# Performance work log

Measured on AMD Instinct MI355X. Metric: run time of the kernel, lower is better.

The kernel has to match this reference:

```python
import jax, jax.numpy as jnp
import numpy as np

DELAY = 4
SKIP = 2
NF = 8
HS = 256
EPS = 1e-5


def setup_inputs() -> dict:
    key = jax.random.key(0)
    ks = jax.random.split(key, 11)
    B, NP, NO, T = 16, 512, 512, 2048
    predictor = jax.random.normal(ks[0], (B, NP, T), dtype=jnp.float32)
    to_order = jax.random.normal(ks[1], (B, NO, T), dtype=jnp.float32)
    trilinear = jax.random.normal(ks[2], (NF, NO, NP), dtype=jnp.float32) / np.float32(np.sqrt(NP * NO))
    w_o = jax.random.normal(ks[3], (HS, NO), dtype=jnp.float32) / np.float32(np.sqrt(NO))
    b_o = jax.random.normal(ks[4], (HS,), dtype=jnp.float32) * 0.01
    w_p = jax.random.normal(ks[5], (HS, NP), dtype=jnp.float32) / np.float32(np.sqrt(NP))
    b_p = jax.random.normal(ks[6], (HS,), dtype=jnp.float32) * 0.01
    bn_gamma = jnp.ones((HS,), dtype=jnp.float32)
    bn_beta = jnp.zeros((HS,), dtype=jnp.float32)
    w_out = jax.random.normal(ks[7], (NF, HS), dtype=jnp.float32) / np.float32(np.sqrt(HS))
    b_out = jax.random.normal(ks[8], (NF,), dtype=jnp.float32) * 0.01
    return {"predictor": predictor, "to_order": to_order, "trilinear": trilinear,
            "w_o": w_o, "b_o": b_o, "w_p": w_p, "b_p": b_p,
            "bn_gamma": bn_gamma, "bn_beta": bn_beta, "w_out": w_out, "b_out": b_out}


def reference(predictor, to_order, trilinear, w_o, b_o, w_p, b_p, bn_gamma, bn_beta, w_out, b_out):
    B, NP, T = predictor.shape
    NO = to_order.shape[1]
    tot_latency = DELAY + SKIP * (NF - 1)
    T_r = T - tot_latency
    pred = predictor[:, :, :T_r]          # (B, np, Tr)
    too = to_order[:, :, DELAY:]          # (B, no, T - delay)
    # predictor_product[b,k,t,m] = sum_p pred[b,p,t] * trilinear[k,m,p]
    pp = jnp.einsum('bpt,kmp->bktm', pred, trilinear)           # (B, nf, Tr, no)
    win = jnp.stack([too[:, :, j * SKIP: j * SKIP + T_r] for j in range(NF)], axis=1)  # (B, nf, no, Tr)
    inner = jnp.einsum('bjmt,bktm->bjkt', win, pp)              # (B, nf, nf, Tr)
    # conv1d (kernel 1) heads
    o_proj = jnp.einsum('hm,bmt->bht', w_o, too) + b_o[None, :, None]    # (B, hs, T - delay)
    p_proj = jnp.einsum('hp,bpt->bht', w_p, pred) + b_p[None, :, None]   # (B, hs, Tr)
    o_win = jnp.stack([o_proj[:, :, j * SKIP: j * SKIP + T_r] for j in range(NF)], axis=1)  # (B, nf, hs, Tr)
    h = jax.nn.relu(o_win + p_proj[:, None])                    # (B, nf, hs, Tr)
    # BatchNorm1d (training-mode batch stats) over (B*nf, hs, Tr): stats over axes (0,1,3)
    mean = h.mean(axis=(0, 1, 3), keepdims=True)
    var = h.var(axis=(0, 1, 3), keepdims=True)
    h = (h - mean) * jax.lax.rsqrt(var + EPS) * bn_gamma[None, None, :, None] + bn_beta[None, None, :, None]
    head = jnp.einsum('kh,bjht->bjkt', w_out, h) + b_out[None, None, :, None]
    inner = inner + head
    log_probs = jax.nn.log_softmax(inner, axis=2)               # (B, nf, nf, Tr)
    correct = jnp.einsum('bjjt->bjt', log_probs)                # diagonal j == k
    return correct.mean(axis=2).mean(axis=0)                    # (nf,)
```

## Files before the change

### kernel.cpp

```cpp
#include <hip/hip_runtime.h>
#include <math.h>

constexpr int B_  = 16;
constexpr int NP_ = 512;
constexpr int NO_ = 512;
constexpr int T_  = 2048;
constexpr int NF_ = 8;
constexpr int HS_ = 256;
constexpr int TR_ = 2030;
constexpr int TO_ = 2044;
constexpr int OPLD_ = 2048;
constexpr float EPS_ = 1e-5f;

typedef short bf16x8 __attribute__((ext_vector_type(8)));
typedef float f32x16 __attribute__((ext_vector_type(16)));

__device__ __forceinline__ unsigned short f2bf(float f) {
  union { float f; unsigned int u; } v; v.f = f;
  unsigned int r = v.u + 0x7fffu + ((v.u >> 16) & 1u);
  return (unsigned short)(r >> 16);
}
__device__ __forceinline__ float bf2f(unsigned short u) {
  union { unsigned int u; float f; } v; v.u = ((unsigned int)u) << 16;
  return v.f;
}

typedef const __attribute__((address_space(1))) unsigned int* gas_u32;
typedef __attribute__((address_space(3))) unsigned int* las_u32;
__device__ __forceinline__ void gl16(const void* g, void* l) {
  __builtin_amdgcn_global_load_lds((gas_u32)g, (las_u32)l, 16, 0, 0);
}


__global__ __launch_bounds__(256) void transpose_cvt(
    const float* __restrict__ in, unsigned short* __restrict__ outb) {
  __shared__ float tile[64][65];
  const int c0 = blockIdx.x * 64;
  const int r0 = blockIdx.y * 64;
  const int b  = blockIdx.z;
  const float* ib = in + (size_t)b * 512 * 2048;
  unsigned short* ob = outb + (size_t)b * 2048 * 512;
  for (int i = threadIdx.x; i < 64 * 16; i += 256) {
    const int r = i >> 4, c4 = (i & 15) * 4;
    float4 v = *(const float4*)(ib + (size_t)(r0 + r) * 2048 + c0 + c4);
    tile[r][c4 + 0] = v.x; tile[r][c4 + 1] = v.y;
    tile[r][c4 + 2] = v.z; tile[r][c4 + 3] = v.w;
  }
  __syncthreads();
  for (int i = threadIdx.x; i < 64 * 8; i += 256) {
    const int c = i >> 3, r8 = (i & 7) * 8;
    unsigned int pk[4];
    #pragma unroll
    for (int e = 0; e < 4; ++e)
      pk[e] = (unsigned int)f2bf(tile[r8 + 2 * e][c]) |
              ((unsigned int)f2bf(tile[r8 + 2 * e + 1][c]) << 16);
    *(uint4*)(ob + (size_t)(c0 + c) * 512 + r0 + r8) = *(uint4*)pk;
  }
}

__global__ __launch_bounds__(256) void cvt_bf16(
    const float* __restrict__ in, unsigned short* __restrict__ out, int n) {
  const int i = (blockIdx.x * 256 + threadIdx.x) * 4;
  if (i < n) {
    float4 v = *(const float4*)(in + i);
    ushort4 o; o.x = f2bf(v.x); o.y = f2bf(v.y); o.z = f2bf(v.z); o.w = f2bf(v.w);
    *(ushort4*)(out + i) = o;
  }
}

__global__ __launch_bounds__(256, 2) void proj_mfma(
    const unsigned short* __restrict__ Wbf,
    const unsigned short* __restrict__ Xt,
    const float* __restrict__ bias,
    unsigned short* __restrict__ out,
    int Tlen, int toff) {
  __shared__ char smem[65536];
  char* const Ab[2] = { smem, smem + 16384 };
  char* const Bb[2] = { smem + 32768, smem + 49152 };
  const int tid = threadIdx.x;
  const int l = tid & 63, wv = tid >> 6;
  const int h = l >> 5, tl = l & 31;
  const int mq = wv >> 1, tq = wv & 1;
  const int t0 = blockIdx.x * 128;
  const int m0 = blockIdx.y * 128;
  const int b  = blockIdx.z;
  const unsigned short* Xb = Xt + (size_t)b * T_ * 512;

  int aSrc[4], bSrc[4], ldsO[4];
  #pragma unroll
  for (int i = 0; i < 4; ++i) {
    const int q = (wv << 8) + (i << 6) + l;
    const int r = q >> 3, c8s = (q & 7) ^ (r & 7);
    aSrc[i] = (m0 + r) * 512 + (c8s << 3);
    const int row = min(t0 + toff + r, T_ - 1);
    bSrc[i] = row * 512 + (c8s << 3);
    ldsO[i] = ((wv << 8) + (i << 6)) << 4;
  }

  f32x16 acc[2][2];
  #pragma unroll
  for (int i = 0; i < 2; ++i)
    #pragma unroll
    for (int jj = 0; jj < 2; ++jj)
      #pragma unroll
      for (int e = 0; e < 16; ++e) acc[i][jj][e] = 0.f;

  #pragma unroll
  for (int i = 0; i < 4; ++i) gl16(Wbf + aSrc[i], Ab[0] + ldsO[i]);
  #pragma unroll
  for (int i = 0; i < 4; ++i) gl16(Xb + bSrc[i], Bb[0] + ldsO[i]);
  asm volatile("s_waitcnt vmcnt(0)" ::: "memory");
  __builtin_amdgcn_s_barrier();

  #pragma unroll
  for (int ps = 0; ps < 8; ++ps) {
    const int cb = ps & 1;
    if (ps < 7) {
      const int p0 = (ps + 1) << 6;
      #pragma unroll
      for (int i = 0; i < 4; ++i) gl16(Wbf + p0 + aSrc[i], Ab[cb ^ 1] + ldsO[i]);
      #pragma unroll
      for (int i = 0; i < 4; ++i) gl16(Xb + p0 + bSrc[i], Bb[cb ^ 1] + ldsO[i]);
    }
    const unsigned short* As = (const unsigned short*)Ab[cb];
    const unsigned short* Bs = (const unsigned short*)Bb[cb];
    #pragma unroll
    for (int s = 0; s < 4; ++s) {
      const int k8 = 2 * s + h;
      bf16x8 af[2], bfr[2];
      #pragma unroll
      for (int mt = 0; mt < 2; ++mt) {
        const int rm = 64 * mq + 32 * mt + tl;
        af[mt] = *(const bf16x8*)(As + rm * 64 + ((k8 ^ (rm & 7)) << 3));
      }
      #pragma unroll
      for (int nt = 0; nt < 2; ++nt) {
        const int rt = 64 * tq + 32 * nt + tl;
        bfr[nt] = *(const bf16x8*)(Bs + rt * 64 + ((k8 ^ (rt & 7)) << 3));
      }
      #pragma unroll
      for (int mt = 0; mt < 2; ++mt)
        #pragma unroll
        for (int nt = 0; nt < 2; ++nt)
          acc[mt][nt] = __builtin_amdgcn_mfma_f32_32x32x16_bf16(
              af[mt], bfr[nt], acc[mt][nt], 0, 0, 0);
    }
    asm volatile("s_waitcnt vmcnt(0)" ::: "memory");
    __builtin_amdgcn_s_barrier();
  }
  #pragma unroll
  for (int mt = 0; mt < 2; ++mt)
    #pragma unroll
    for (int nt = 0; nt < 2; ++nt)
      #pragma unroll
      for (int r = 0; r < 16; ++r) {
        const int hs = m0 + 64 * mq + 32 * mt + (r & 3) + 8 * (r >> 2) + 4 * h;
        const int t  = t0 + 64 * tq + 32 * nt + tl;
        if (t < Tlen)
          out[((size_t)b * HS_ + hs) * OPLD_ + t] = f2bf(acc[mt][nt][r] + bias[hs]);
      }
}

__global__ __launch_bounds__(256, 2) void inner_mfma(
    const unsigned short* __restrict__ pred_t,
    const unsigned short* __restrict__ too_t,
    const unsigned short* __restrict__ tri_bf,
    float* __restrict__ inner) {
  __shared__ char smem[77824];
  char* const Pb[2] = { smem, smem + 16384 };
  char* const Tb[2] = { smem + 32768, smem + 49152 };
  char* const TOOM  = smem + 65536;
  char* const TAIL  = smem + 32768;
  const int tid = threadIdx.x;
  const int l = tid & 63, wv = tid >> 6;
  const int h = l >> 5, tl = l & 31;
  const int mh = wv & 1, th = wv >> 1;
  const int t0 = blockIdx.x * 128;
  const int kf0 = blockIdx.y * 2;
  const int b  = blockIdx.z;
  const unsigned short* predB = pred_t + (size_t)b * T_ * NP_;
  const unsigned short* tooB  = too_t  + (size_t)b * T_ * NO_;
  const unsigned short* triK  = tri_bf + (size_t)kf0 * NO_ * NP_;

  int pSrc[4], pLds[4];
  #pragma unroll
  for (int i = 0; i < 4; ++i) {
    const int q = (wv << 8) + (i << 6) + l;
    const int r = q >> 3, c8s = (q & 7) ^ (r & 7);
    pSrc[i] = (t0 + r) * NP_ + (c8s << 3);
    pLds[i] = ((wv << 8) + (i << 6)) << 4;
  }
  int tSrc[4], tLds[4];
  #pragma unroll
  for (int i = 0; i < 4; ++i) {
    const int q = (wv << 8) + (i << 6) + l;
    const int f = q >> 9, qq = q & 511;
    const int r = qq >> 3, c8s = (qq & 7) ^ (r & 7);
    tSrc[i] = f * (NO_ * NP_) + r * NP_ + (c8s << 3);
    tLds[i] = ((wv << 8) + (i << 6)) << 4;
  }
  int oSrc[3], oLds[3];
  #pragma unroll
  for (int i = 0; i < 3; ++i) {
    const int q = wv * 192 + (i << 6) + l;
    const int r = q >> 3, c8s = (q & 7) ^ (r & 7);
    oSrc[i] = (t0 + r) * NO_ + (c8s << 3);
    oLds[i] = (wv * 192 + (i << 6)) << 4;
  }
  int aSrcT[4], aLdsT[4];
  {
    const int ws = (wv >= 2) ? (wv - 2) : 0;
    #pragma unroll
    for (int i = 0; i < 4; ++i) {
      const int q = (ws << 8) + (i << 6) + l;
      const int r = 96 + (q >> 3), c8s = (q & 7) ^ (r & 7);
      aSrcT[i] = min(t0 + r, T_ - 1) * NO_ + (c8s << 3);
      aLdsT[i] = ((ws << 8) + (i << 6)) << 4;
    }
  }

  f32x16 Sacc[2][2];
  #pragma unroll
  for (int f = 0; f < 2; ++f)
    #pragma unroll
    for (int ct = 0; ct < 2; ++ct)
      #pragma unroll
      for (int e = 0; e < 16; ++e) Sacc[f][ct][e] = 0.f;

  for (int mc = 0; mc < 8; ++mc) {
    const int m0 = mc << 6;
    const int mOff = m0 * NP_;
    __builtin_amdgcn_s_barrier();
    #pragma unroll
    for (int i = 0; i < 3; ++i) gl16(tooB + m0 + oSrc[i], TOOM + oLds[i]);
    #pragma unroll
    for (int i = 0; i < 4; ++i) gl16(triK + mOff + tSrc[i], Tb[0] + tLds[i]);
    #pragma unroll
    for (int i = 0; i < 4; ++i) gl16(predB + pSrc[i], Pb[0] + pLds[i]);
    asm volatile("s_waitcnt vmcnt(0)" ::: "memory");
    __builtin_amdgcn_s_barrier();

    f32x16 Qacc[2][2];
    #pragma unroll
    for (int f = 0; f < 2; ++f)
      #pragma unroll
      for (int nt = 0; nt < 2; ++nt)
        #pragma unroll
        for (int e = 0; e < 16; ++e) Qacc[f][nt][e] = 0.f;

    #pragma unroll
    for (int ps = 0; ps < 8; ++ps) {
      const int cb = ps & 1;
      if (ps < 7) {
        const int p1 = (ps + 1) << 6;
        #pragma unroll
        for (int i = 0; i < 4; ++i)
          gl16(triK + mOff + p1 + tSrc[i], Tb[cb ^ 1] + tLds[i]);
        #pragma unroll
        for (int i = 0; i < 4; ++i)
          gl16(predB + p1 + pSrc[i], Pb[cb ^ 1] + pLds[i]);
      }
      const unsigned short* predS = (const unsigned short*)Pb[cb];
      const unsigned short* triS  = (const unsigned short*)Tb[cb];
      __builtin_amdgcn_s_setprio(1);
      #pragma unroll
      for (int s = 0; s < 4; ++s) {
        const int k8 = 2 * s + h;
        const int swz = (k8 ^ (tl & 7)) << 3;
        bf16x8 a[2], bp[2];
        #pragma unroll
        for (int f = 0; f < 2; ++f)
          a[f] = *(const bf16x8*)(triS + f * 4096 + ((mh << 5) + tl) * 64 + swz);
        #pragma unroll
        for (int nt = 0; nt < 2; ++nt)
          bp[nt] = *(const bf16x8*)(predS + ((th << 6) + (nt << 5) + tl) * 64 + swz);
        #pragma unroll
        for (int f = 0; f < 2; ++f)
          #pragma unroll
          for (int nt = 0; nt < 2; ++nt)
            Qacc[f][nt] = __builtin_amdgcn_mfma_f32_32x32x16_bf16(
                a[f], bp[nt], Qacc[f][nt], 0, 0, 0);
      }
      __builtin_amdgcn_s_setprio(0);
      if (ps == 7 && wv >= 2) {
        #pragma unroll
        for (int i = 0; i < 4; ++i)
          gl16(tooB + m0 + aSrcT[i], TAIL + aLdsT[i]);
      }
      asm volatile("s_waitcnt vmcnt(0)" ::: "memory");
      __builtin_amdgcn_s_barrier();
    }
    #pragma unroll
    for (int f = 0; f < 2; ++f)
      #pragma unroll
      for (int nt = 0; nt < 2; ++nt) {
        unsigned short* QSw = (unsigned short*)(Pb[f] + (((th << 1) + nt) << 12));
        #pragma unroll
        for (int rp = 0; rp < 8; ++rp) {
          const int r = rp << 1;
          const int m = (mh << 5) + (r & 3) + ((r >> 2) << 3) + (h << 2);
          const int c8 = m >> 3, ml = m & 7;
          const int rX = (tl & 24) | ((tl ^ c8) & 7);
          const unsigned int pk = (unsigned int)f2bf(Qacc[f][nt][r]) |
                                  ((unsigned int)f2bf(Qacc[f][nt][r + 1]) << 16);
          *(unsigned int*)(QSw + (((c8 << 5) + rX) << 3) + ml) = pk;
        }
      }
    asm volatile("s_waitcnt lgkmcnt(0)" ::: "memory");
    __builtin_amdgcn_s_barrier();
    #pragma unroll
    for (int s = 0; s < 4; ++s) {
      const int k8 = 2 * s + h;
      bf16x8 atoo[2];
      #pragma unroll
      for (int ct = 0; ct < 2; ++ct) {
        const int rbase = (wv + ct) << 5;
        const int rr = rbase + tl;
        const unsigned short* tb = (rbase < 96)
            ? (const unsigned short*)TOOM + (size_t)rr * 64
            : (const unsigned short*)TAIL + (size_t)(rr - 96) * 64;
        atoo[ct] = *(const bf16x8*)(tb + ((k8 ^ (rr & 7)) << 3));
      }
      const int rqX = (tl & 24) | ((tl ^ k8) & 7);
      #pragma unroll
      for (int f = 0; f < 2; ++f) {
        const bf16x8 bq = *(const bf16x8*)((const unsigned short*)(Pb[f] + (wv << 12)) +
                                           (((k8 << 5) + rqX) << 3));
        #pragma unroll
        for (int ct = 0; ct < 2; ++ct)
          Sacc[f][ct] = __builtin_amdgcn_mfma_f32_32x32x16_bf16(atoo[ct], bq, Sacc[f][ct], 0, 0, 0);
      }
    }
  }
  __syncthreads();
  const int tglob = t0 + (wv << 5) + tl;
  float* SW = (float*)smem + (wv << 11);
  #pragma unroll
  for (int f = 0; f < 2; ++f) {
    #pragma unroll
    for (int ct = 0; ct < 2; ++ct)
      #pragma unroll
      for (int r = 0; r < 16; ++r) {
        const int cc = (ct << 5) + (r & 3) + ((r >> 2) << 3) + (h << 2);
        SW[(cc << 5) + tl] = Sacc[f][ct][r];
      }
    if (tglob < TR_) {
      #pragma unroll
      for (int jj = 0; jj < 4; ++jj) {
        const int j = (jj << 1) + h;
        const float v = SW[((tl + 4 + 2 * j) << 5) + tl];
        inner[(((size_t)b * NF_ + j) * NF_ + (kf0 + f)) * TR_ + tglob] = v;
      }
    }
  }
}

__global__ __launch_bounds__(256) void bn_stats(
    const unsigned short* __restrict__ op, const unsigned short* __restrict__ pp,
    float* __restrict__ partials) {
  const int hh = blockIdx.x, b = blockIdx.y;
  const unsigned short* oprow = op + ((size_t)b * HS_ + hh) * OPLD_;
  const unsigned short* pprow = pp + ((size_t)b * HS_ + hh) * OPLD_;
  float s = 0.f, s2 = 0.f;
  const int t8 = threadIdx.x * 8;
  if (t8 < TR_) {
    uint4 pv4 = *(const uint4*)(pprow + t8);
    uint4 ov[3];
    ov[0] = *(const uint4*)(oprow + t8);
    ov[1] = *(const uint4*)(oprow + t8 + 8);
    ov[2] = *(const uint4*)(oprow + t8 + 16);
    float ppf[8], opf[24];
    #pragma unroll
    for (int i = 0; i < 4; ++i) {
      const unsigned int u = (&pv4.x)[i];
      ppf[2 * i]     = bf2f((unsigned short)(u & 0xffffu));
      ppf[2 * i + 1] = bf2f((unsigned short)(u >> 16));
    }
    #pragma unroll
    for (int g = 0; g < 3; ++g)
      #pragma unroll
      for (int i = 0; i < 4; ++i) {
        const unsigned int u = (&ov[g].x)[i];
        opf[8 * g + 2 * i]     = bf2f((unsigned short)(u & 0xffffu));
        opf[8 * g + 2 * i + 1] = bf2f((unsigned short)(u >> 16));
      }
    #pragma unroll
    for (int e = 0; e < 8; ++e) {
      if (t8 + e < TR_) {
        #pragma unroll
        for (int j = 0; j < NF_; ++j) {
          float r = fmaxf(opf[e + 2 * j] + ppf[e], 0.f);
          s += r; s2 += r * r;
        }
      }
    }
  }
  __shared__ float red[256], red2[256];
  red[threadIdx.x] = s; red2[threadIdx.x] = s2;
  __syncthreads();
  for (int st = 128; st > 0; st >>= 1) {
    if (threadIdx.x < st) {
      red[threadIdx.x]  += red[threadIdx.x + st];
      red2[threadIdx.x] += red2[threadIdx.x + st];
    }
    __syncthreads();
  }
  if (threadIdx.x == 0) {
    partials[b * HS_ + hh]            = red[0];
    partials[B_ * HS_ + b * HS_ + hh] = red2[0];
  }
}

__global__ __launch_bounds__(256) void bn_finalize(
    const float* __restrict__ partials, const float* __restrict__ gamma,
    const float* __restrict__ beta, const float* __restrict__ w_out,
    const float* __restrict__ b_out, float* __restrict__ w_eff,
    float* __restrict__ cvec) {
  const int hh = threadIdx.x;
  float s = 0.f, s2 = 0.f;
  for (int b = 0; b < B_; ++b) {
    s  += partials[b * HS_ + hh];
    s2 += partials[B_ * HS_ + b * HS_ + hh];
  }
  const float cnt  = (float)B_ * NF_ * TR_;
  const float mean = s / cnt;
  const float var  = s2 / cnt - mean * mean;
  const float scale = gamma[hh] * rsqrtf(var + EPS_);
  const float shift = beta[hh] - mean * scale;
  #pragma unroll
  for (int k = 0; k < NF_; ++k) w_eff[k * HS_ + hh] = w_out[k * HS_ + hh] * scale;
  __shared__ float red[256];
  for (int k = 0; k < NF_; ++k) {
    red[hh] = w_out[k * HS_ + hh] * shift;
    __syncthreads();
    for (int st = 128; st > 0; st >>= 1) {
      if (hh < st) red[hh] += red[hh + st];
      __syncthreads();
    }
    if (hh == 0) cvec[k] = b_out[k] + red[0];
    __syncthreads();
  }
}

__global__ __launch_bounds__(256) void head_final(
    const unsigned short* __restrict__ op, const unsigned short* __restrict__ pp,
    const float* __restrict__ w_eff, const float* __restrict__ cvec,
    const float* __restrict__ inner, float* __restrict__ part3) {
  __shared__ float opS[144 * 20];
  __shared__ float ppS[128 * 20];
  __shared__ float weS[8][256];
  __shared__ float red[4][2];
  const int tid = threadIdx.x;
  const int tl = tid & 127, jp = tid >> 7;
  const int t0 = blockIdx.x * 128;
  const int b  = blockIdx.y;
  const int jh = blockIdx.z;
  for (int i = tid; i < 8 * 256; i += 256) weS[i >> 8][i & 255] = w_eff[i];
  float acc[2][8] = {};
  const unsigned short* opb = op + (size_t)b * HS_ * OPLD_;
  const unsigned short* ppb = pp + (size_t)b * HS_ * OPLD_;
  for (int hc = 0; hc < 16; ++hc) {
    const int h0 = hc << 4;
    __syncthreads();
    for (int idx = tid; idx < 288; idx += 256) {
      const int r = idx / 18, cc = (idx - r * 18) << 3;
      const int g = min(t0 + cc, OPLD_ - 8);
      uint4 v = *(const uint4*)(opb + (size_t)(h0 + r) * OPLD_ + g);
      #pragma unroll
      for (int e = 0; e < 4; ++e) {
        const unsigned int u = (&v.x)[e];
        opS[(cc + 2 * e) * 20 + r]     = bf2f((unsigned short)(u & 0xffffu));
        opS[(cc + 2 * e + 1) * 20 + r] = bf2f((unsigned short)(u >> 16));
      }
    }
    {
      const int r = tid >> 4, cc = (tid & 15) << 3;
      uint4 v = *(const uint4*)(ppb + (size_t)(h0 + r) * OPLD_ + t0 + cc);
      #pragma unroll
      for (int e = 0; e < 4; ++e) {
        const unsigned int u = (&v.x)[e];
        ppS[(cc + 2 * e) * 20 + r]     = bf2f((unsigned short)(u & 0xffffu));
        ppS[(cc + 2 * e + 1) * 20 + r] = bf2f((unsigned short)(u >> 16));
      }
    }
    __syncthreads();
    float pv[16];
    #pragma unroll
    for (int i = 0; i < 4; ++i) {
      float4 q = *(const float4*)(ppS + tl * 20 + 4 * i);
      pv[4 * i + 0] = q.x; pv[4 * i + 1] = q.y;
      pv[4 * i + 2] = q.z; pv[4 * i + 3] = q.w;
    }
    #pragma unroll
    for (int jj = 0; jj < 2; ++jj) {
      const int col = tl + 2 * ((jh << 2) + (jp << 1) + jj);
      #pragma unroll
      for (int i = 0; i < 4; ++i) {
        float4 ov = *(const float4*)(opS + col * 20 + 4 * i);
        #pragma unroll
        for (int e = 0; e < 4; ++e) {
          const float r = fmaxf((&ov.x)[e] + pv[4 * i + e], 0.f);
          #pragma unroll
          for (int k = 0; k < 8; ++k) acc[jj][k] += weS[k][h0 + 4 * i + e] * r;
        }
      }
    }
  }
  const int t = t0 + tl;
  float sj[2];
  #pragma unroll
  for (int jj = 0; jj < 2; ++jj) {
    if (t < TR_) {
      const int j = (jh << 2) + (jp << 1) + jj;
      float v[8]; float mx = -1e30f;
      #pragma unroll
      for (int k = 0; k < 8; ++k) {
        v[k] = acc[jj][k] + cvec[k] +
               inner[(((size_t)b * NF_ + j) * NF_ + k) * TR_ + t];
        mx = fmaxf(mx, v[k]);
      }
      float se = 0.f;
      #pragma unroll
      for (int k = 0; k < 8; ++k) se += expf(v[k] - mx);
      sj[jj] = v[j] - mx - logf(se);
    } else sj[jj] = 0.f;
  }
  #pragma unroll
  for (int jj = 0; jj < 2; ++jj)
    #pragma unroll
    for (int off = 32; off > 0; off >>= 1) sj[jj] += __shfl_down(sj[jj], off);
  if ((tid & 63) == 0) {
    const int wv = tid >> 6;
    #pragma unroll
    for (int jj = 0; jj < 2; ++jj) red[wv][jj] = sj[jj];
  }
  __syncthreads();
  if (tid < 4) {
    const int qp = tid >> 1, qj = tid & 1;
    const float s = red[2 * qp][qj] + red[2 * qp + 1][qj];
    const int j = (jh << 2) + (qp << 1) + qj;
    part3[(j * B_ + b) * 16 + blockIdx.x] = s;
  }
}

__global__ void final_out(const float* __restrict__ part3, float* __restrict__ out) {
  const int j = threadIdx.x;
  if (j < NF_) {
    float s = 0.f;
    for (int i = 0; i < B_ * 16; ++i) s += part3[j * B_ * 16 + i];
    out[j] = s / ((float)B_ * (float)TR_);
  }
}

extern "C" void kernel_launch(void* const* d_in, const int* in_sizes, int n_in,
                              void* d_out, int out_size, void* d_ws, size_t ws_size,
                              hipStream_t stream) {
  const float* predictor = (const float*)d_in[0];
  const float* to_order  = (const float*)d_in[1];
  const float* trilinear = (const float*)d_in[2];
  const float* w_o   = (const float*)d_in[3];
  const float* b_o   = (const float*)d_in[4];
  const float* w_p   = (const float*)d_in[5];
  const float* b_p   = (const float*)d_in[6];
  const float* bn_g  = (const float*)d_in[7];
  const float* bn_b  = (const float*)d_in[8];
  const float* w_out = (const float*)d_in[9];
  const float* b_out = (const float*)d_in[10];
  float* out = (float*)d_out;

  char* w = (char*)d_ws;
  unsigned short* pred_t = (unsigned short*)w; w += (size_t)B_ * T_ * NP_ * 2;
  unsigned short* too_t  = (unsigned short*)w; w += (size_t)B_ * T_ * NO_ * 2;
  unsigned short* tri_bf = (unsigned short*)w; w += (size_t)NF_ * NO_ * NP_ * 2;
  unsigned short* wo_bf  = (unsigned short*)w; w += (size_t)HS_ * NO_ * 2;
  unsigned short* wp_bf  = (unsigned short*)w; w += (size_t)HS_ * NP_ * 2;
  unsigned short* o_proj = (unsigned short*)w; w += (size_t)B_ * HS_ * OPLD_ * 2;
  unsigned short* p_proj = (unsigned short*)w; w += (size_t)B_ * HS_ * OPLD_ * 2;
  float* inner    = (float*)w; w += (size_t)B_ * NF_ * NF_ * TR_ * 4;
  float* partials = (float*)w; w += (size_t)2 * B_ * HS_ * 4;
  float* w_eff    = (float*)w; w += (size_t)NF_ * HS_ * 4;
  float* cvec     = (float*)w; w += 256;
  float* part3    = (float*)w; w += (size_t)NF_ * B_ * 16 * 4;

  transpose_cvt<<<dim3(32, 8, 16), 256, 0, stream>>>(predictor, pred_t);
  transpose_cvt<<<dim3(32, 8, 16), 256, 0, stream>>>(to_order, too_t);
  cvt_bf16<<<2048, 256, 0, stream>>>(trilinear, tri_bf, NF_ * NO_ * NP_);
  cvt_bf16<<<128, 256, 0, stream>>>(w_o, wo_bf, HS_ * NO_);
  cvt_bf16<<<128, 256, 0, stream>>>(w_p, wp_bf, HS_ * NP_);

  proj_mfma<<<dim3(16, 2, 16), 256, 0, stream>>>(wo_bf, too_t, b_o, o_proj, TO_, 4);
  proj_mfma<<<dim3(16, 2, 16), 256, 0, stream>>>(wp_bf, pred_t, b_p, p_proj, TR_, 0);

  inner_mfma<<<dim3(16, 4, 16), 256, 0, stream>>>(pred_t, too_t, tri_bf, inner);

  bn_stats<<<dim3(HS_, B_), 256, 0, stream>>>(o_proj, p_proj, partials);
  bn_finalize<<<1, 256, 0, stream>>>(partials, bn_g, bn_b, w_out, b_out, w_eff, cvec);
  head_final<<<dim3(16, B_, 2), 256, 0, stream>>>(o_proj, p_proj, w_eff, cvec, inner, part3);
  final_out<<<1, 64, 0, stream>>>(part3, out);
}
```

Baseline: 349.5 us.

## Merge transpose and projection launches, halve head_final tile, drop setprio

Merges the two transpose_cvt launches into one grid with z selecting the input, and the two proj_mfma launches into one grid with blockIdx.y selecting the o or p projection. This removes launch gaps and gives each launch more blocks. head_final now uses 64-wide time tiles with one j per wave instead of two, doubling the grid so more blocks run on the GPU, with the partial-sum layout widened to match. The s_setprio hints around the inner_mfma MFMA loop are removed. The head change adds redundant op/pp tile loads across blocks.

```diff
diff --git a/kernel.cpp b/kernel.cpp
--- a/kernel.cpp
+++ b/kernel.cpp
@@ -33,13 +33,15 @@
 
 
 __global__ __launch_bounds__(256) void transpose_cvt(
-    const float* __restrict__ in, unsigned short* __restrict__ outb) {
+    const float* __restrict__ inA, unsigned short* __restrict__ outA,
+    const float* __restrict__ inB, unsigned short* __restrict__ outB) {
   __shared__ float tile[64][65];
   const int c0 = blockIdx.x * 64;
   const int r0 = blockIdx.y * 64;
-  const int b  = blockIdx.z;
-  const float* ib = in + (size_t)b * 512 * 2048;
-  unsigned short* ob = outb + (size_t)b * 2048 * 512;
+  const int z  = blockIdx.z;
+  const int b  = z & 15;
+  const float* ib = ((z < 16) ? inA : inB) + (size_t)b * 512 * 2048;
+  unsigned short* ob = ((z < 16) ? outA : outB) + (size_t)b * 2048 * 512;
   for (int i = threadIdx.x; i < 64 * 16; i += 256) {
     const int r = i >> 4, c4 = (i & 15) * 4;
     float4 v = *(const float4*)(ib + (size_t)(r0 + r) * 2048 + c0 + c4);
@@ -69,20 +71,26 @@
 }
 
 __global__ __launch_bounds__(256, 2) void proj_mfma(
-    const unsigned short* __restrict__ Wbf,
-    const unsigned short* __restrict__ Xt,
-    const float* __restrict__ bias,
-    unsigned short* __restrict__ out,
-    int Tlen, int toff) {
+    const unsigned short* __restrict__ Wo, const unsigned short* __restrict__ Wp,
+    const unsigned short* __restrict__ Xo, const unsigned short* __restrict__ Xp,
+    const float* __restrict__ biasO, const float* __restrict__ biasP,
+    unsigned short* __restrict__ outO, unsigned short* __restrict__ outP) {
   __shared__ char smem[65536];
   char* const Ab[2] = { smem, smem + 16384 };
   char* const Bb[2] = { smem + 32768, smem + 49152 };
+  const int sel = blockIdx.y >> 1;
+  const unsigned short* Wbf = sel ? Wp : Wo;
+  const unsigned short* Xt  = sel ? Xp : Xo;
+  const float* bias = sel ? biasP : biasO;
+  unsigned short* out = sel ? outP : outO;
+  const int Tlen = sel ? TR_ : TO_;
+  const int toff = sel ? 0 : 4;
   const int tid = threadIdx.x;
   const int l = tid & 63, wv = tid >> 6;
   const int h = l >> 5, tl = l & 31;
   const int mq = wv >> 1, tq = wv & 1;
   const int t0 = blockIdx.x * 128;
-  const int m0 = blockIdx.y * 128;
+  const int m0 = (blockIdx.y & 1) * 128;
   const int b  = blockIdx.z;
   const unsigned short* Xb = Xt + (size_t)b * T_ * 512;
 
@@ -262,7 +270,6 @@
       }
       const unsigned short* predS = (const unsigned short*)Pb[cb];
       const unsigned short* triS  = (const unsigned short*)Tb[cb];
-      __builtin_amdgcn_s_setprio(1);
       #pragma unroll
       for (int s = 0; s < 4; ++s) {
         const int k8 = 2 * s + h;
@@ -281,7 +288,6 @@
             Qacc[f][nt] = __builtin_amdgcn_mfma_f32_32x32x16_bf16(
                 a[f], bp[nt], Qacc[f][nt], 0, 0, 0);
       }
-      __builtin_amdgcn_s_setprio(0);
       if (ps == 7 && wv >= 2) {
         #pragma unroll
         for (int i = 0; i < 4; ++i)
@@ -446,24 +452,25 @@
     const unsigned short* __restrict__ op, const unsigned short* __restrict__ pp,
     const float* __restrict__ w_eff, const float* __restrict__ cvec,
     const float* __restrict__ inner, float* __restrict__ part3) {
-  __shared__ float opS[144 * 20];
-  __shared__ float ppS[128 * 20];
+  __shared__ float opS[80 * 20];
+  __shared__ float ppS[64 * 20];
   __shared__ float weS[8][256];
-  __shared__ float red[4][2];
+  __shared__ float red[4];
   const int tid = threadIdx.x;
-  const int tl = tid & 127, jp = tid >> 7;
-  const int t0 = blockIdx.x * 128;
+  const int tl = tid & 63, jp = tid >> 6;
+  const int t0 = blockIdx.x * 64;
   const int b  = blockIdx.y;
   const int jh = blockIdx.z;
+  const int j  = (jh << 2) + jp;
   for (int i = tid; i < 8 * 256; i += 256) weS[i >> 8][i & 255] = w_eff[i];
-  float acc[2][8] = {};
+  float acc[8] = {};
   const unsigned short* opb = op + (size_t)b * HS_ * OPLD_;
   const unsigned short* ppb = pp + (size_t)b * HS_ * OPLD_;
   for (int hc = 0; hc < 16; ++hc) {
     const int h0 = hc << 4;
     __syncthreads();
-    for (int idx = tid; idx < 288; idx += 256) {
-      const int r = idx / 18, cc = (idx - r * 18) << 3;
+    if (tid < 160) {
+      const int r = tid / 10, cc = (tid - r * 10) << 3;
       const int g = min(t0 + cc, OPLD_ - 8);
       uint4 v = *(const uint4*)(opb + (size_t)(h0 + r) * OPLD_ + g);
       #pragma unroll
@@ -473,8 +480,8 @@
         opS[(cc + 2 * e + 1) * 20 + r] = bf2f((unsigned short)(u >> 16));
       }
     }
-    {
-      const int r = tid >> 4, cc = (tid & 15) << 3;
+    if (tid < 128) {
+      const int r = tid >> 3, cc = (tid & 7) << 3;
       uint4 v = *(const uint4*)(ppb + (size_t)(h0 + r) * OPLD_ + t0 + cc);
       #pragma unroll
       for (int e = 0; e < 4; ++e) {
@@ -491,55 +498,40 @@
       pv[4 * i + 0] = q.x; pv[4 * i + 1] = q.y;
       pv[4 * i + 2] = q.z; pv[4 * i + 3] = q.w;
     }
-    #pragma unroll
-    for (int jj = 0; jj < 2; ++jj) {
-      const int col = tl + 2 * ((jh << 2) + (jp << 1) + jj);
-      #pragma unroll
-      for (int i = 0; i < 4; ++i) {
-        float4 ov = *(const float4*)(opS + col * 20 + 4 * i);
-        #pragma unroll
-        for (int e = 0; e < 4; ++e) {
-          const float r = fmaxf((&ov.x)[e] + pv[4 * i + e], 0.f);
-          #pragma unroll
-          for (int k = 0; k < 8; ++k) acc[jj][k] += weS[k][h0 + 4 * i + e] * r;
-        }
+    const int col = tl + 2 * j;
+    #pragma unroll
+    for (int i = 0; i < 4; ++i) {
+      float4 ov = *(const float4*)(opS + col * 20 + 4 * i);
+      #pragma unroll
+      for (int e = 0; e < 4; ++e) {
+        const float r = fmaxf((&ov.x)[e] + pv[4 * i + e], 0.f);
+        #pragma unroll
+        for (int k = 0; k < 8; ++k) acc[k] += weS[k][h0 + 4 * i + e] * r;
       }
     }
   }
   const int t = t0 + tl;
-  float sj[2];
-  #pragma unroll
-  for (int jj = 0; jj < 2; ++jj) {
-    if (t < TR_) {
-      const int j = (jh << 2) + (jp << 1) + jj;
-      float v[8]; float mx = -1e30f;
-      #pragma unroll
-      for (int k = 0; k < 8; ++k) {
-        v[k] = acc[jj][k] + cvec[k] +
-               inner[(((size_t)b * NF_ + j) * NF_ + k) * TR_ + t];
-        mx = fmaxf(mx, v[k]);
-      }
-      float se = 0.f;
-      #pragma unroll
-      for (int k = 0; k < 8; ++k) se += expf(v[k] - mx);
-      sj[jj] = v[j] - mx - logf(se);
-    } else sj[jj] = 0.f;
-  }
-  #pragma unroll
-  for (int jj = 0; jj < 2; ++jj)
-    #pragma unroll
-    for (int off = 32; off > 0; off >>= 1) sj[jj] += __shfl_down(sj[jj], off);
-  if ((tid & 63) == 0) {
-    const int wv = tid >> 6;
-    #pragma unroll
-    for (int jj = 0; jj < 2; ++jj) red[wv][jj] = sj[jj];
-  }
+  float sj = 0.f;
+  if (t < TR_) {
+    float v[8]; float mx = -1e30f;
+    #pragma unroll
+    for (int k = 0; k < 8; ++k) {
+      v[k] = acc[k] + cvec[k] +
+             inner[(((size_t)b * NF_ + j) * NF_ + k) * TR_ + t];
+      mx = fmaxf(mx, v[k]);
+    }
+    float se = 0.f;
+    #pragma unroll
+    for (int k = 0; k < 8; ++k) se += expf(v[k] - mx);
+    sj = v[j] - mx - logf(se);
+  }
+  #pragma unroll
+  for (int off = 32; off > 0; off >>= 1) sj += __shfl_down(sj, off);
+  if ((tid & 63) == 0) red[jp] = sj;
   __syncthreads();
   if (tid < 4) {
-    const int qp = tid >> 1, qj = tid & 1;
-    const float s = red[2 * qp][qj] + red[2 * qp + 1][qj];
-    const int j = (jh << 2) + (qp << 1) + qj;
-    part3[(j * B_ + b) * 16 + blockIdx.x] = s;
+    const int jw = (jh << 2) + tid;
+    part3[(jw * B_ + b) * 32 + blockIdx.x] = red[tid];
   }
 }
 
@@ -547,7 +539,7 @@
   const int j = threadIdx.x;
   if (j < NF_) {
     float s = 0.f;
-    for (int i = 0; i < B_ * 16; ++i) s += part3[j * B_ * 16 + i];
+    for (int i = 0; i < B_ * 32; ++i) s += part3[j * B_ * 32 + i];
     out[j] = s / ((float)B_ * (float)TR_);
   }
 }
@@ -580,21 +572,21 @@
   float* partials = (float*)w; w += (size_t)2 * B_ * HS_ * 4;
   float* w_eff    = (float*)w; w += (size_t)NF_ * HS_ * 4;
   float* cvec     = (float*)w; w += 256;
-  float* part3    = (float*)w; w += (size_t)NF_ * B_ * 16 * 4;
-
-  transpose_cvt<<<dim3(32, 8, 16), 256, 0, stream>>>(predictor, pred_t);
-  transpose_cvt<<<dim3(32, 8, 16), 256, 0, stream>>>(to_order, too_t);
+  float* part3    = (float*)w; w += (size_t)NF_ * B_ * 32 * 4;
+
+  transpose_cvt<<<dim3(32, 8, 32), 256, 0, stream>>>(predictor, pred_t,
+                                                     to_order, too_t);
   cvt_bf16<<<2048, 256, 0, stream>>>(trilinear, tri_bf, NF_ * NO_ * NP_);
   cvt_bf16<<<128, 256, 0, stream>>>(w_o, wo_bf, HS_ * NO_);
   cvt_bf16<<<128, 256, 0, stream>>>(w_p, wp_bf, HS_ * NP_);
 
-  proj_mfma<<<dim3(16, 2, 16), 256, 0, stream>>>(wo_bf, too_t, b_o, o_proj, TO_, 4);
-  proj_mfma<<<dim3(16, 2, 16), 256, 0, stream>>>(wp_bf, pred_t, b_p, p_proj, TR_, 0);
+  proj_mfma<<<dim3(16, 4, 16), 256, 0, stream>>>(
+      wo_bf, wp_bf, too_t, pred_t, b_o, b_p, o_proj, p_proj);
 
   inner_mfma<<<dim3(16, 4, 16), 256, 0, stream>>>(pred_t, too_t, tri_bf, inner);
 
   bn_stats<<<dim3(HS_, B_), 256, 0, stream>>>(o_proj, p_proj, partials);
   bn_finalize<<<1, 256, 0, stream>>>(partials, bn_g, bn_b, w_out, b_out, w_eff, cvec);
-  head_final<<<dim3(16, B_, 2), 256, 0, stream>>>(o_proj, p_proj, w_eff, cvec, inner, part3);
+  head_final<<<dim3(32, B_, 2), 256, 0, stream>>>(o_proj, p_proj, w_eff, cvec, inner, part3);
   final_out<<<1, 64, 0, stream>>>(part3, out);
 }
```

Measured after the change: 338.0 us. 3.3% less time.
